# Performance work log

Measured on AMD Instinct MI355X. Metric: run time of the kernel, lower is better.

The kernel has to match this reference:

```python
import jax, jax.numpy as jnp
import numpy as np


def _lstm_cell(x, h, c, Wih, Whh, b):
    # PyTorch gate order: i, f, g, o
    g = x @ Wih.T + h @ Whh.T + b
    i, f, gg, o = jnp.split(g, 4, axis=-1)
    c2 = jax.nn.sigmoid(f) * c + jax.nn.sigmoid(i) * jnp.tanh(gg)
    h2 = jax.nn.sigmoid(o) * jnp.tanh(c2)
    return h2, c2


def _lstm_seq(x_tbd, h0, c0, Wih, Whh, b):
    # x_tbd: [T, B, D] -> outputs [T, B, H]
    def step(carry, xt):
        h, c = carry
        h2, c2 = _lstm_cell(xt, h, c, Wih, Whh, b)
        return (h2, c2), h2
    _, ys = jax.lax.scan(step, (h0, c0), x_tbd)
    return ys


def setup_inputs() -> dict:
    key = jax.random.key(0)
    ks = jax.random.split(key, 20)
    H, D, A, HOR, NQ = 256, 32, 128, 24, 3
    B, T = 256, 512
    s = 0.1
    inp = {
        'x':      jax.random.normal(ks[0], (B, T, D), jnp.float32),
        'e_Wih0': jax.random.normal(ks[1], (4 * H, D), jnp.float32) * s,
        'e_Whh0': jax.random.normal(ks[2], (4 * H, H), jnp.float32) * s,
        'e_b0':   jax.random.normal(ks[3], (4 * H,), jnp.float32) * s,
        'e_Wih1': jax.random.normal(ks[4], (4 * H, H), jnp.float32) * s,
        'e_Whh1': jax.random.normal(ks[5], (4 * H, H), jnp.float32) * s,
        'e_b1':   jax.random.normal(ks[6], (4 * H,), jnp.float32) * s,
        'd_Wih0': jax.random.normal(ks[7], (4 * H, 1), jnp.float32) * s,
        'd_Whh0': jax.random.normal(ks[8], (4 * H, H), jnp.float32) * s,
        'd_b0':   jax.random.normal(ks[9], (4 * H,), jnp.float32) * s,
        'd_Wih1': jax.random.normal(ks[10], (4 * H, H), jnp.float32) * s,
        'd_Whh1': jax.random.normal(ks[11], (4 * H, H), jnp.float32) * s,
        'd_b1':   jax.random.normal(ks[12], (4 * H,), jnp.float32) * s,
        'aW':     jax.random.normal(ks[13], (H, A), jnp.float32) * s,
        'aV':     jax.random.normal(ks[14], (A,), jnp.float32) * s,
        'qW':     jax.random.normal(ks[15], (NQ, HOR, H), jnp.float32) * s,
        'qb':     jax.random.normal(ks[16], (NQ, HOR), jnp.float32) * s,
    }
    return inp


def reference(x, e_Wih0, e_Whh0, e_b0, e_Wih1, e_Whh1, e_b1,
              d_Wih0, d_Whh0, d_b0, d_Wih1, d_Whh1, d_b1,
              aW, aV, qW, qb):
    B = x.shape[0]
    H = e_Whh0.shape[1]
    horizon = qW.shape[1]

    # ---- encoder: 2-layer LSTM over time ----
    xt = jnp.swapaxes(x, 0, 1)                      # [T, B, D]
    z = jnp.zeros((B, H), x.dtype)
    h1 = _lstm_seq(xt, z, z, e_Wih0, e_Whh0, e_b0)  # [T, B, H]
    h2 = _lstm_seq(h1, z, z, e_Wih1, e_Whh1, e_b1)  # [T, B, H]
    enc = jnp.swapaxes(h2, 0, 1)                    # [B, T, H]

    # ---- attention over encoder outputs ----
    energy = jnp.tanh(enc @ aW) @ aV                # [B, T]
    w = jax.nn.softmax(energy, axis=1)
    context = jnp.einsum('bt,bth->bh', w, enc)      # [B, H]

    inp0 = x[:, -1, -1:]                            # [B, 1]

    def dstep(carry, _):
        h0_, c0_, h1_, c1_, dinp = carry
        h0n, c0n = _lstm_cell(dinp, h0_, c0_, d_Wih0, d_Whh0, d_b0)
        h1n, c1n = _lstm_cell(h0n, h1_, c1_, d_Wih1, d_Whh1, d_b1)
        return (h0n, c0n, h1n, c1n, h1n[:, :1]), h1n

    _, douts = jax.lax.scan(dstep, (context, context, context, context, inp0),
                            None, length=horizon)   # [horizon, B, H]

    # ---- quantile heads on last decoder step ----
    last = douts[-1]                                # [B, H]
    preds = jnp.einsum('bh,qoh->bqo', last, qW) + qb  # [B, n_quantiles, horizon]
    return preds
```

## Files before the change

### kernel.cpp

```cpp
#include <hip/hip_runtime.h>

typedef unsigned short u16;
typedef unsigned int u32;
typedef unsigned long long u64;
typedef short v8s __attribute__((ext_vector_type(8)));
typedef float v4f __attribute__((ext_vector_type(4)));


__device__ __forceinline__ float bf2f(u16 u) { union { u32 u; float f; } c; c.u = ((u32)u) << 16; return c.f; }
__device__ __forceinline__ u16 f2bf(float f) {
  union { float f; u32 u; } c; c.f = f;
  u32 r = c.u + 0x7FFFu + ((c.u >> 16) & 1u);
  return (u16)(r >> 16);
}
__device__ __forceinline__ float sigf(float x) { return 1.f / (1.f + __expf(-x)); }
__device__ __forceinline__ float tanhfast(float x) {
  x = fminf(15.f, fmaxf(-15.f, x));
  float e = __expf(2.f * x);
  return (e - 1.f) / (e + 1.f);
}
__device__ __forceinline__ float ldIn(const void* p, size_t i, int isbf) {
  return isbf ? bf2f(((const u16*)p)[i]) : ((const float*)p)[i];
}
__device__ __forceinline__ v8s ld8hi(const void* p, size_t e, int isbf) {
  if (isbf) return *(const v8s*)((const u16*)p + e);
  const float* f = (const float*)p + e;
  v8s r;
#pragma unroll
  for (int j = 0; j < 8; ++j) r[j] = (short)f2bf(f[j]);
  return r;
}
__device__ __forceinline__ void ld8split(const void* p, size_t e, int isbf, v8s& hi, v8s& lo) {
  if (isbf) {
    hi = *(const v8s*)((const u16*)p + e);
    lo = v8s{0, 0, 0, 0, 0, 0, 0, 0};
  } else {
    const float* f = (const float*)p + e;
#pragma unroll
    for (int j = 0; j < 8; ++j) {
      u16 h = f2bf(f[j]);
      hi[j] = (short)h;
      lo[j] = (short)f2bf(f[j] - bf2f(h));
    }
  }
}
#define MFMA(a, b, c) __builtin_amdgcn_mfma_f32_16x16x32_bf16(a, b, c, 0, 0, 0)

__device__ __forceinline__ u64 aload64(const u64* p) {
  return __hip_atomic_load(p, __ATOMIC_RELAXED, __HIP_MEMORY_SCOPE_AGENT);
}
__device__ __forceinline__ void astore32(u32* p, u32 v) {
  __hip_atomic_store(p, v, __ATOMIC_RELAXED, __HIP_MEMORY_SCOPE_AGENT);
}
__device__ __forceinline__ void astore64(u64* p, u64 v) {
  __hip_atomic_store(p, v, __ATOMIC_RELAXED, __HIP_MEMORY_SCOPE_AGENT);
}

__device__ __forceinline__ void stage_issue(u64* v, const u32* src, int tid) {
  const u64* p = (const u64*)src;
#pragma unroll
  for (int i = 0; i < 8; ++i) v[i] = aload64(p + i * 256 + tid);
}
__device__ __forceinline__ void stage_finish(u16* dst, const u32* src, u64* v, int tid, u32 tag) {
  const u64* p = (const u64*)src;
  bool all;
  do {
    all = true;
#pragma unroll
    for (int i = 0; i < 8; ++i) {
      u64 w = v[i];
      if (!((((w >> 16) & 0xFFFFull) == tag) && ((w >> 48) == tag))) {
        all = false;
        v[i] = aload64(p + i * 256 + tid);
      }
    }
  } while (!all);
#pragma unroll
  for (int i = 0; i < 8; ++i) {
    int idx = i * 256 + tid;
    int row = (idx >> 3) & 15;
    int jp  = ((idx >> 7) << 3) | (idx & 7);
    u64 w = v[i];
    u32 val = (u32)(w & 0xFFFF) | ((((u32)(w >> 32)) & 0xFFFF) << 16);
    *(u32*)(dst + row * 264 + ((jp * 2) ^ ((row & 7) << 3))) = val;
  }
}

__device__ __forceinline__ void stage_dec(u16* dhi, u16* dlo, const u64* src,
                                          int tid, u32 tag) {
  u64 v[16];
#pragma unroll
  for (int i = 0; i < 16; ++i) v[i] = aload64(src + i * 256 + tid);
  bool all;
  do {
    all = true;
#pragma unroll
    for (int i = 0; i < 16; ++i) {
      if ((u32)(v[i] >> 32) != tag) { all = false; v[i] = aload64(src + i * 256 + tid); }
    }
  } while (!all);
#pragma unroll
  for (int i = 0; i < 16; ++i) {
    int idx = i * 256 + tid;
    int row = idx >> 8, col = idx & 255;
    dhi[row * 264 + col] = (u16)v[i];
    dlo[row * 264 + col] = (u16)(v[i] >> 16);
  }
}
__device__ __forceinline__ void stage_f32(u16* dhi, u16* dlo, const float* src, int tid) {
#pragma unroll
  for (int i = 0; i < 8; ++i) {
    int e = i * 512 + tid * 2;
    int row = e >> 8, jc = e & 255;
    float f0 = src[row * 256 + jc], f1 = src[row * 256 + jc + 1];
    u16 h0 = f2bf(f0), h1 = f2bf(f1);
    u16 l0 = f2bf(f0 - bf2f(h0)), l1 = f2bf(f1 - bf2f(h1));
    ((u32*)(dhi + row * 264))[jc >> 1] = (u32)h0 | ((u32)h1 << 16);
    ((u32*)(dlo + row * 264))[jc >> 1] = (u32)l0 | ((u32)l1 << 16);
  }
}

__global__ void sniff_kernel(const u16* __restrict__ w, int* __restrict__ flag) {
  __shared__ int cnt;
  if (threadIdx.x == 0) cnt = 0;
  __syncthreads();
  int ok = 0;
  for (int i = threadIdx.x; i < 1024; i += 256) {
    u16 u = w[2 * i];
    int e = (u >> 7) & 0xFF;
    ok += (u == 0 || (e >= 97 && e <= 140)) ? 1 : 0;
  }
  atomicAdd(&cnt, ok);
  __syncthreads();
  if (threadIdx.x == 0) *flag = (cnt >= 768) ? 1 : 0;
}

__global__ __launch_bounds__(256, 1) void enc_kernel(
    const void* __restrict__ x,
    const void* __restrict__ eWih0, const void* __restrict__ eWhh0, const void* __restrict__ eb0,
    const void* __restrict__ eWih1, const void* __restrict__ eWhh1, const void* __restrict__ eb1,
    const void* __restrict__ aW, const void* __restrict__ aV,
    u32* __restrict__ H0, u32* __restrict__ H1,
    float* __restrict__ ctx, const int* __restrict__ flagp) {
  __shared__ __align__(16) u16 h0s[16 * 264], h1s[16 * 264];
  __shared__ float gb0[16 * 66], gb1[16 * 66];
  __shared__ float eP[16 * 132];

  const int isbf = *flagp;
  const int tid = threadIdx.x, blk = blockIdx.x;
  const int grp = blk & 15, gs = blk >> 4;
  const int lane = tid & 63, wv = tid >> 6;
  const int ln = lane & 15, lq = lane >> 4;

  v8s W0F[9], W1F[16], AWF[16];
  {
    const int gw = wv * 256 + gs * 16 + ln;
    const int kq = lq * 8;
    W0F[0] = ld8hi(eWih0, (size_t)gw * 32 + kq, isbf);
#pragma unroll
    for (int kt = 0; kt < 8; ++kt) {
      W0F[kt + 1] = ld8hi(eWhh0, (size_t)gw * 256 + kt * 32 + kq, isbf);
      W1F[kt]     = ld8hi(eWhh1, (size_t)gw * 256 + kt * 32 + kq, isbf);
      W1F[kt + 8] = ld8hi(eWih1, (size_t)gw * 256 + kt * 32 + kq, isbf);
    }
#pragma unroll
    for (int kt = 0; kt < 8; ++kt)
#pragma unroll
      for (int j2 = 0; j2 < 2; ++j2) {
        v8s f;
        int ac = (2 * wv + j2) * 16 + ln;
#pragma unroll
        for (int j = 0; j < 8; ++j)
          f[j] = (short)f2bf(ldIn(aW, (size_t)(kt * 32 + kq + j) * 128 + ac, isbf));
        AWF[kt * 2 + j2] = f;
      }
  }

  const int urow = tid >> 4, uu = tid & 15;
  float bg0[4], bg1[4], aVr[8];
#pragma unroll
  for (int g = 0; g < 4; ++g) {
    bg0[g] = ldIn(eb0, g * 256 + gs * 16 + uu, isbf);
    bg1[g] = ldIn(eb1, g * 256 + gs * 16 + uu, isbf);
  }
#pragma unroll
  for (int j = 0; j < 8; ++j) aVr[j] = ldIn(aV, (size_t)(uu + 16 * j), isbf);

  const int gRowU = grp * 16 + urow;
  const int gUnit = gs * 16 + uu;
  const int aRow = grp * 16 + ln;
  const u32 stOff = (u32)(grp * 4096 + gs * 256 + urow * 16 + uu);

  float c0 = 0.f, c1 = 0.f;
  float mS = -3e38f, lS = 0.f, ctxA = 0.f;

  v8s xh_c, xl_c;
  ld8split(x, ((size_t)aRow * 512) * 32 + lq * 8, isbf, xh_c, xl_c);

  u64 v0s[8];
  stage_issue(v0s, H0 + (size_t)1 * 65536 + grp * 4096, tid);
  v8s a0r[8];

#pragma unroll 1
  for (int t = 0; t < 514; ++t) {
    const int rB = (t + 1) & 1, wB = t & 1;
    const u32 tag = (u32)(u16)t;
    if (t <= 512)
      stage_finish(h0s, H0 + (size_t)rB * 65536 + grp * 4096, v0s, tid, tag);
    __syncthreads();

    if (t <= 512) {
#pragma unroll
      for (int kt = 0; kt < 8; ++kt)
        a0r[kt] = *(const v8s*)(h0s + ln * 264 + ((kt * 32 + lq * 8) ^ ((ln & 7) << 3)));
    }
    if (t < 512) {
      v4f acc0 = {0, 0, 0, 0};
      acc0 = MFMA(xh_c, W0F[0], acc0);
      if (!isbf) acc0 = MFMA(xl_c, W0F[0], acc0);
#pragma unroll
      for (int kt = 0; kt < 8; ++kt) acc0 = MFMA(a0r[kt], W0F[kt + 1], acc0);
#pragma unroll
      for (int r = 0; r < 4; ++r) gb0[(lq * 4 + r) * 66 + wv * 16 + ln] = acc0[r];
    }
    __syncthreads();

    u64 v1s[8];
    stage_issue(v1s, H1 + (size_t)wB * 65536 + grp * 4096, tid);
    const u32 tagS = (u32)(u16)(t + 1) << 16;
    if (t < 512) {
      float gi = gb0[urow * 66 + uu]      + bg0[0];
      float gf = gb0[urow * 66 + 16 + uu] + bg0[1];
      float gg = gb0[urow * 66 + 32 + uu] + bg0[2];
      float go = gb0[urow * 66 + 48 + uu] + bg0[3];
      c0 = sigf(gf) * c0 + sigf(gi) * tanhfast(gg);
      float h = sigf(go) * tanhfast(c0);
      astore32(H0 + (size_t)wB * 65536 + stOff, (u32)f2bf(h) | tagS);
    }
    stage_finish(h1s, H1 + (size_t)wB * 65536 + grp * 4096, v1s, tid, tag);
    __syncthreads();

    v4f acc1 = {0, 0, 0, 0}, accA0 = {0, 0, 0, 0}, accA1 = {0, 0, 0, 0};
#pragma unroll
    for (int kt = 0; kt < 8; ++kt) {
      v8s a1 = *(const v8s*)(h1s + ln * 264 + ((kt * 32 + lq * 8) ^ ((ln & 7) << 3)));
      acc1 = MFMA(a0r[kt], W1F[kt + 8], acc1);
      acc1 = MFMA(a1, W1F[kt], acc1);
      accA0 = MFMA(a1, AWF[kt * 2], accA0);
      accA1 = MFMA(a1, AWF[kt * 2 + 1], accA1);
    }
#pragma unroll
    for (int r = 0; r < 4; ++r) {
      gb1[(lq * 4 + r) * 66 + wv * 16 + ln] = acc1[r];
      eP[(lq * 4 + r) * 132 + (2 * wv) * 16 + ln] = accA0[r];
      eP[(lq * 4 + r) * 132 + (2 * wv + 1) * 16 + ln] = accA1[r];
    }
    v8s xh_n, xl_n;
    {
      int tn = (t + 1 < 512) ? t + 1 : 511;
      ld8split(x, ((size_t)aRow * 512 + tn) * 32 + lq * 8, isbf, xh_n, xl_n);
    }
    __syncthreads();

    if (t >= 1 && t < 513) {
      float gi = gb1[urow * 66 + uu]      + bg1[0];
      float gf = gb1[urow * 66 + 16 + uu] + bg1[1];
      float gg = gb1[urow * 66 + 32 + uu] + bg1[2];
      float go = gb1[urow * 66 + 48 + uu] + bg1[3];
      c1 = sigf(gf) * c1 + sigf(gi) * tanhfast(gg);
      float h = sigf(go) * tanhfast(c1);
      astore32(H1 + (size_t)rB * 65536 + stOff, (u32)f2bf(h) | tagS);
    } else if (t == 0) {
      astore32(H1 + (size_t)rB * 65536 + stOff, tagS);
    }
    if (t + 1 <= 512)
      stage_issue(v0s, H0 + (size_t)((t + 2) & 1) * 65536 + grp * 4096, tid);
    if (t >= 2) {
      float h1v = bf2f(h1s[urow * 264 + (gUnit ^ ((urow & 7) << 3))]);
      float e = 0.f;
#pragma unroll
      for (int j = 0; j < 8; ++j)
        e += tanhfast(eP[urow * 132 + uu + 16 * j]) * aVr[j];
      e += __shfl_xor(e, 1);
      e += __shfl_xor(e, 2);
      e += __shfl_xor(e, 4);
      e += __shfl_xor(e, 8);
      float nm = fmaxf(mS, e);
      float al = __expf(mS - nm), p = __expf(e - nm);
      lS = lS * al + p;
      ctxA = ctxA * al + p * h1v;
      mS = nm;
    }
    xh_c = xh_n; xl_c = xl_n;
  }
  ctx[(size_t)gRowU * 256 + gUnit] = ctxA / lS;
}

__global__ __launch_bounds__(256, 1) void dec_kernel(
    const void* __restrict__ x,
    const void* __restrict__ dWih0, const void* __restrict__ dWhh0, const void* __restrict__ db0,
    const void* __restrict__ dWih1, const void* __restrict__ dWhh1, const void* __restrict__ db1,
    const void* __restrict__ qW, const void* __restrict__ qb,
    const float* __restrict__ ctx,
    u64* __restrict__ H0d, u64* __restrict__ H1d, u64* __restrict__ dinpG,
    void* __restrict__ out, const int* __restrict__ flagp) {
  __shared__ u16 sAhi[16 * 264], sAlo[16 * 264], sBhi[16 * 264], sBlo[16 * 264];
  __shared__ float gb[16 * 64];
  __shared__ float dinpS[16];

  const int isbf = *flagp;
  const int tid = threadIdx.x, blk = blockIdx.x;
  const int grp = blk & 15, gs = blk >> 4;
  const int lane = tid & 63, wv = tid >> 6;
  const int ln = lane & 15, lq = lane >> 4;

  v8s W0F[8], W1F[16];
  {
    const int gw = wv * 256 + gs * 16 + ln;
    const int kq = lq * 8;
#pragma unroll
    for (int kt = 0; kt < 8; ++kt) {
      W0F[kt]     = ld8hi(dWhh0, (size_t)gw * 256 + kt * 32 + kq, isbf);
      W1F[kt]     = ld8hi(dWhh1, (size_t)gw * 256 + kt * 32 + kq, isbf);
      W1F[kt + 8] = ld8hi(dWih1, (size_t)gw * 256 + kt * 32 + kq, isbf);
    }
  }
  const int urow = tid >> 4, uu = tid & 15;
  float bg0[4], bg1[4], w0v[4];
#pragma unroll
  for (int g = 0; g < 4; ++g) {
    bg0[g] = ldIn(db0, g * 256 + gs * 16 + uu, isbf);
    bg1[g] = ldIn(db1, g * 256 + gs * 16 + uu, isbf);
    w0v[g] = ldIn(dWih0, g * 256 + gs * 16 + uu, isbf);
  }
  const int gRowU = grp * 16 + urow;
  const int gUnit = gs * 16 + uu;

  float c0 = ctx[(size_t)gRowU * 256 + gUnit];
  float c1 = c0;

#pragma unroll 1
  for (int t = 0; t < 24; ++t) {
    const int pPrev = (t + 1) & 1, pCur = t & 1;
    if (t == 0) {
      stage_f32(sAhi, sAlo, ctx + (size_t)grp * 16 * 256, tid);
      if (tid < 16)
        dinpS[tid] = ldIn(x, ((size_t)(grp * 16 + tid) * 512 + 511) * 32 + 31, isbf);
    } else {
      stage_dec(sAhi, sAlo, H0d + (size_t)pPrev * 65536 + grp * 4096, tid, (u32)(2 * t - 1));
      if (tid < 16) {
        u64 w;
        do { w = aload64(dinpG + pPrev * 256 + grp * 16 + tid); } while ((u32)(w >> 32) != (u32)(2 * t));
        dinpS[tid] = __uint_as_float((u32)w);
      }
    }
    __syncthreads();
    v4f acc = {0, 0, 0, 0};
#pragma unroll
    for (int kt = 0; kt < 8; ++kt) {
      const int off = ln * 264 + kt * 32 + lq * 8;
      acc = MFMA(*(const v8s*)(sAhi + off), W0F[kt], acc);
      acc = MFMA(*(const v8s*)(sAlo + off), W0F[kt], acc);
    }
    {
      const int bR = lq * 4;
#pragma unroll
      for (int r = 0; r < 4; ++r) gb[(bR + r) * 64 + ln * 4 + wv] = acc[r];
    }
    float di = dinpS[urow];
    __syncthreads();
    {
      const float* g0 = gb + (urow * 16 + uu) * 4;
      float gi = g0[0] + bg0[0] + di * w0v[0];
      float gf = g0[1] + bg0[1] + di * w0v[1];
      float gg = g0[2] + bg0[2] + di * w0v[2];
      float go = g0[3] + bg0[3] + di * w0v[3];
      c0 = sigf(gf) * c0 + sigf(gi) * tanhfast(gg);
      float h = sigf(go) * tanhfast(c0);
      u16 hh = f2bf(h); u16 hl = f2bf(h - bf2f(hh));
      astore64(H0d + (size_t)pCur * 65536 + gRowU * 256 + gUnit,
               (u64)hh | ((u64)hl << 16) | ((u64)(u32)(2 * t + 1) << 32));
    }
    if (t == 0) stage_f32(sBhi, sBlo, ctx + (size_t)grp * 16 * 256, tid);
    else stage_dec(sBhi, sBlo, H1d + (size_t)pPrev * 65536 + grp * 4096, tid, (u32)(2 * t));
    stage_dec(sAhi, sAlo, H0d + (size_t)pCur * 65536 + grp * 4096, tid, (u32)(2 * t + 1));
    __syncthreads();
    v4f a1 = {0, 0, 0, 0};
#pragma unroll
    for (int kt = 0; kt < 8; ++kt) {
      const int off = ln * 264 + kt * 32 + lq * 8;
      a1 = MFMA(*(const v8s*)(sBhi + off), W1F[kt], a1);
      a1 = MFMA(*(const v8s*)(sBlo + off), W1F[kt], a1);
      a1 = MFMA(*(const v8s*)(sAhi + off), W1F[kt + 8], a1);
      a1 = MFMA(*(const v8s*)(sAlo + off), W1F[kt + 8], a1);
    }
    {
      const int bR = lq * 4;
#pragma unroll
      for (int r = 0; r < 4; ++r) gb[(bR + r) * 64 + ln * 4 + wv] = a1[r];
    }
    __syncthreads();
    {
      const float* g1 = gb + (urow * 16 + uu) * 4;
      float gi = g1[0] + bg1[0], gf = g1[1] + bg1[1], gg = g1[2] + bg1[2], go = g1[3] + bg1[3];
      c1 = sigf(gf) * c1 + sigf(gi) * tanhfast(gg);
      float h = sigf(go) * tanhfast(c1);
      u16 hh = f2bf(h); u16 hl = f2bf(h - bf2f(hh));
      astore64(H1d + (size_t)pCur * 65536 + gRowU * 256 + gUnit,
               (u64)hh | ((u64)hl << 16) | ((u64)(u32)(2 * t + 2) << 32));
      if (gUnit == 0)
        astore64(dinpG + pCur * 256 + gRowU,
                 (u64)__float_as_uint(h) | ((u64)(u32)(2 * t + 2) << 32));
    }
  }
  stage_dec(sAhi, sAlo, H1d + (size_t)65536 + grp * 4096, tid, 48u);
  __syncthreads();
  if (gs < 12 && tid < 96) {
    int r = tid / 6, p = tid % 6;
    int qo = gs * 6 + p, row = grp * 16 + r;
    float s = ldIn(qb, qo, isbf);
    for (int h = 0; h < 256; ++h)
      s += (bf2f(sAhi[r * 264 + h]) + bf2f(sAlo[r * 264 + h])) * ldIn(qW, (size_t)qo * 256 + h, isbf);
    if (isbf) ((u16*)out)[row * 72 + qo] = f2bf(s);
    else      ((float*)out)[row * 72 + qo] = s;
  }
}

extern "C" void kernel_launch(void* const* d_in, const int* in_sizes, int n_in,
                              void* d_out, int out_size, void* d_ws, size_t ws_size,
                              hipStream_t stream) {
  const void* x     = d_in[0];
  const void* eWih0 = d_in[1];
  const void* eWhh0 = d_in[2];
  const void* eb0   = d_in[3];
  const void* eWih1 = d_in[4];
  const void* eWhh1 = d_in[5];
  const void* eb1   = d_in[6];
  const void* dWih0 = d_in[7];
  const void* dWhh0 = d_in[8];
  const void* db0   = d_in[9];
  const void* dWih1 = d_in[10];
  const void* dWhh1 = d_in[11];
  const void* db1   = d_in[12];
  const void* aW    = d_in[13];
  const void* aV    = d_in[14];
  const void* qW    = d_in[15];
  const void* qb    = d_in[16];

  char* wsb = (char*)d_ws;
  u32*   H0    = (u32*)(wsb + 0);
  u32*   H1    = (u32*)(wsb + 524288);
  int*   flag  = (int*)(wsb + 1048576);
  float* ctx   = (float*)(wsb + 1048832);
  u64*   dinpG = (u64*)(wsb + 1310976);
  u64*   H0d   = (u64*)(wsb + 1315072);
  u64*   H1d   = (u64*)(wsb + 2363648);

  hipMemsetAsync(wsb, 0, 1048576, stream);

  sniff_kernel<<<1, 256, 0, stream>>>((const u16*)eWhh0, flag);
  enc_kernel<<<256, 256, 0, stream>>>(x, eWih0, eWhh0, eb0, eWih1, eWhh1, eb1,
                                      aW, aV, H0, H1, ctx, flag);
  dec_kernel<<<256, 256, 0, stream>>>(x, dWih0, dWhh0, db0, dWih1, dWhh1, db1,
                                      qW, qb, ctx, H0d, H1d, dinpG,
                                      d_out, flag);
}
```

Baseline: 2.270 ms.

## Add per-block progress tag counters for encoder inter-block polling

Blocks now publish a per-group progress counter after consuming each step. Before loading a step's hidden state, consumers spin on 16 tag words with a wave-wide vote instead of repeatedly reloading the full 8-word tagged buffer. The early prefetch (issue before the barrier) of H0 is dropped, and the LDS layouts of hidden-state and gate buffers change: the XOR swizzle is removed and gates are interleaved so each thread reads its four gates contiguously. This aims to cut wasted polling traffic and simplify indexing, at the cost of an extra polling round trip per stage, possible LDS bank conflicts without the swizzle, and the decoder workspace now aliasing the encoder buffers.

```diff
diff --git a/kernel.cpp b/kernel.cpp
--- a/kernel.cpp
+++ b/kernel.cpp
@@ -49,6 +49,9 @@
 __device__ __forceinline__ u64 aload64(const u64* p) {
   return __hip_atomic_load(p, __ATOMIC_RELAXED, __HIP_MEMORY_SCOPE_AGENT);
 }
+__device__ __forceinline__ u32 aload32(const u32* p) {
+  return __hip_atomic_load(p, __ATOMIC_RELAXED, __HIP_MEMORY_SCOPE_AGENT);
+}
 __device__ __forceinline__ void astore32(u32* p, u32 v) {
   __hip_atomic_store(p, v, __ATOMIC_RELAXED, __HIP_MEMORY_SCOPE_AGENT);
 }
@@ -56,12 +59,17 @@
   __hip_atomic_store(p, v, __ATOMIC_RELAXED, __HIP_MEMORY_SCOPE_AGENT);
 }
 
-__device__ __forceinline__ void stage_issue(u64* v, const u32* src, int tid) {
+__device__ __forceinline__ void poll16(const u32* tl, int lane, u32 tag) {
+  u32 s = aload32(tl + (lane & 15));
+  while (!__all(s >= tag)) s = aload32(tl + (lane & 15));
+}
+__device__ __forceinline__ void load8(u64* v, const u32* src, int tid) {
   const u64* p = (const u64*)src;
 #pragma unroll
   for (int i = 0; i < 8; ++i) v[i] = aload64(p + i * 256 + tid);
 }
-__device__ __forceinline__ void stage_finish(u16* dst, const u32* src, u64* v, int tid, u32 tag) {
+__device__ __forceinline__ void verify_unpack(u16* dst, const u32* src, u64* v,
+                                              int tid, u32 tag) {
   const u64* p = (const u64*)src;
   bool all;
   do {
@@ -78,11 +86,10 @@
 #pragma unroll
   for (int i = 0; i < 8; ++i) {
     int idx = i * 256 + tid;
-    int row = (idx >> 3) & 15;
-    int jp  = ((idx >> 7) << 3) | (idx & 7);
+    int gs2 = idx >> 7, row = (idx >> 3) & 15, c = idx & 7;
     u64 w = v[i];
-    u32 val = (u32)(w & 0xFFFF) | ((((u32)(w >> 32)) & 0xFFFF) << 16);
-    *(u32*)(dst + row * 264 + ((jp * 2) ^ ((row & 7) << 3))) = val;
+    ((u32*)(dst + row * 264))[gs2 * 8 + c] =
+        (u32)(w & 0xFFFF) | ((((u32)(w >> 32)) & 0xFFFF) << 16);
   }
 }
 
@@ -141,9 +148,10 @@
     const void* __restrict__ eWih1, const void* __restrict__ eWhh1, const void* __restrict__ eb1,
     const void* __restrict__ aW, const void* __restrict__ aV,
     u32* __restrict__ H0, u32* __restrict__ H1,
+    u32* __restrict__ H0tag, u32* __restrict__ H1tag,
     float* __restrict__ ctx, const int* __restrict__ flagp) {
   __shared__ __align__(16) u16 h0s[16 * 264], h1s[16 * 264];
-  __shared__ float gb0[16 * 66], gb1[16 * 66];
+  __shared__ float gb0[16 * 64], gb1[16 * 64];
   __shared__ float eP[16 * 132];
 
   const int isbf = *flagp;
@@ -190,29 +198,34 @@
   const int gUnit = gs * 16 + uu;
   const int aRow = grp * 16 + ln;
   const u32 stOff = (u32)(grp * 4096 + gs * 256 + urow * 16 + uu);
+  const u32* tl0 = H0tag + grp * 32;
+  const u32* tl1 = H1tag + grp * 32;
 
   float c0 = 0.f, c1 = 0.f;
   float mS = -3e38f, lS = 0.f, ctxA = 0.f;
 
   v8s xh_c, xl_c;
   ld8split(x, ((size_t)aRow * 512) * 32 + lq * 8, isbf, xh_c, xl_c);
-
-  u64 v0s[8];
-  stage_issue(v0s, H0 + (size_t)1 * 65536 + grp * 4096, tid);
   v8s a0r[8];
 
 #pragma unroll 1
   for (int t = 0; t < 514; ++t) {
     const int rB = (t + 1) & 1, wB = t & 1;
     const u32 tag = (u32)(u16)t;
-    if (t <= 512)
-      stage_finish(h0s, H0 + (size_t)rB * 65536 + grp * 4096, v0s, tid, tag);
-    __syncthreads();
-
     if (t <= 512) {
+      const u32* src0 = H0 + (size_t)rB * 65536 + grp * 4096;
+      poll16(tl0, lane, (u32)t);
+      u64 v0[8];
+      load8(v0, src0, tid);
+      verify_unpack(h0s, src0, v0, tid, tag);
+    }
+    __syncthreads();
+
+    if (t >= 1 && tid == 0) astore32(H1tag + grp * 32 + gs, (u32)t);
+    if (t <= 512) {
 #pragma unroll
       for (int kt = 0; kt < 8; ++kt)
-        a0r[kt] = *(const v8s*)(h0s + ln * 264 + ((kt * 32 + lq * 8) ^ ((ln & 7) << 3)));
+        a0r[kt] = *(const v8s*)(h0s + ln * 264 + kt * 32 + lq * 8);
     }
     if (t < 512) {
       v4f acc0 = {0, 0, 0, 0};
@@ -221,29 +234,31 @@
 #pragma unroll
       for (int kt = 0; kt < 8; ++kt) acc0 = MFMA(a0r[kt], W0F[kt + 1], acc0);
 #pragma unroll
-      for (int r = 0; r < 4; ++r) gb0[(lq * 4 + r) * 66 + wv * 16 + ln] = acc0[r];
-    }
-    __syncthreads();
-
-    u64 v1s[8];
-    stage_issue(v1s, H1 + (size_t)wB * 65536 + grp * 4096, tid);
+      for (int r = 0; r < 4; ++r) gb0[(lq * 4 + r) * 64 + ln * 4 + wv] = acc0[r];
+    }
+    __syncthreads();
+
+    const u32* src1 = H1 + (size_t)wB * 65536 + grp * 4096;
+    poll16(tl1, lane, (u32)t);
+    u64 v1[8];
+    load8(v1, src1, tid);
     const u32 tagS = (u32)(u16)(t + 1) << 16;
     if (t < 512) {
-      float gi = gb0[urow * 66 + uu]      + bg0[0];
-      float gf = gb0[urow * 66 + 16 + uu] + bg0[1];
-      float gg = gb0[urow * 66 + 32 + uu] + bg0[2];
-      float go = gb0[urow * 66 + 48 + uu] + bg0[3];
+      const float* g0 = gb0 + (urow * 16 + uu) * 4;
+      float gi = g0[0] + bg0[0], gf = g0[1] + bg0[1], gg = g0[2] + bg0[2], go = g0[3] + bg0[3];
       c0 = sigf(gf) * c0 + sigf(gi) * tanhfast(gg);
       float h = sigf(go) * tanhfast(c0);
       astore32(H0 + (size_t)wB * 65536 + stOff, (u32)f2bf(h) | tagS);
     }
-    stage_finish(h1s, H1 + (size_t)wB * 65536 + grp * 4096, v1s, tid, tag);
-    __syncthreads();
-
+    verify_unpack(h1s, src1, v1, tid, tag);
+    float h1v = bf2f(h1s[urow * 264 + gUnit]);
+    __syncthreads();
+
+    if (t < 512 && tid == 0) astore32(H0tag + grp * 32 + gs, (u32)(t + 1));
     v4f acc1 = {0, 0, 0, 0}, accA0 = {0, 0, 0, 0}, accA1 = {0, 0, 0, 0};
 #pragma unroll
     for (int kt = 0; kt < 8; ++kt) {
-      v8s a1 = *(const v8s*)(h1s + ln * 264 + ((kt * 32 + lq * 8) ^ ((ln & 7) << 3)));
+      v8s a1 = *(const v8s*)(h1s + ln * 264 + kt * 32 + lq * 8);
       acc1 = MFMA(a0r[kt], W1F[kt + 8], acc1);
       acc1 = MFMA(a1, W1F[kt], acc1);
       accA0 = MFMA(a1, AWF[kt * 2], accA0);
@@ -251,7 +266,7 @@
     }
 #pragma unroll
     for (int r = 0; r < 4; ++r) {
-      gb1[(lq * 4 + r) * 66 + wv * 16 + ln] = acc1[r];
+      gb1[(lq * 4 + r) * 64 + ln * 4 + wv] = acc1[r];
       eP[(lq * 4 + r) * 132 + (2 * wv) * 16 + ln] = accA0[r];
       eP[(lq * 4 + r) * 132 + (2 * wv + 1) * 16 + ln] = accA1[r];
     }
@@ -263,20 +278,15 @@
     __syncthreads();
 
     if (t >= 1 && t < 513) {
-      float gi = gb1[urow * 66 + uu]      + bg1[0];
-      float gf = gb1[urow * 66 + 16 + uu] + bg1[1];
-      float gg = gb1[urow * 66 + 32 + uu] + bg1[2];
-      float go = gb1[urow * 66 + 48 + uu] + bg1[3];
+      const float* g1 = gb1 + (urow * 16 + uu) * 4;
+      float gi = g1[0] + bg1[0], gf = g1[1] + bg1[1], gg = g1[2] + bg1[2], go = g1[3] + bg1[3];
       c1 = sigf(gf) * c1 + sigf(gi) * tanhfast(gg);
       float h = sigf(go) * tanhfast(c1);
       astore32(H1 + (size_t)rB * 65536 + stOff, (u32)f2bf(h) | tagS);
     } else if (t == 0) {
       astore32(H1 + (size_t)rB * 65536 + stOff, tagS);
     }
-    if (t + 1 <= 512)
-      stage_issue(v0s, H0 + (size_t)((t + 2) & 1) * 65536 + grp * 4096, tid);
     if (t >= 2) {
-      float h1v = bf2f(h1s[urow * 264 + (gUnit ^ ((urow & 7) << 3))]);
       float e = 0.f;
 #pragma unroll
       for (int j = 0; j < 8; ++j)
@@ -450,17 +460,19 @@
   char* wsb = (char*)d_ws;
   u32*   H0    = (u32*)(wsb + 0);
   u32*   H1    = (u32*)(wsb + 524288);
-  int*   flag  = (int*)(wsb + 1048576);
-  float* ctx   = (float*)(wsb + 1048832);
-  u64*   dinpG = (u64*)(wsb + 1310976);
-  u64*   H0d   = (u64*)(wsb + 1315072);
-  u64*   H1d   = (u64*)(wsb + 2363648);
-
-  hipMemsetAsync(wsb, 0, 1048576, stream);
+  u32*   H0tag = (u32*)(wsb + 1048576);
+  u32*   H1tag = (u32*)(wsb + 1050624);
+  int*   flag  = (int*)(wsb + 1052672);
+  float* ctx   = (float*)(wsb + 1052928);
+  u64*   dinpG = (u64*)(wsb + 1315072);
+  u64*   H0d   = (u64*)(wsb + 0);
+  u64*   H1d   = (u64*)(wsb + 1319168);
+
+  hipMemsetAsync(wsb, 0, 1052672, stream);
 
   sniff_kernel<<<1, 256, 0, stream>>>((const u16*)eWhh0, flag);
   enc_kernel<<<256, 256, 0, stream>>>(x, eWih0, eWhh0, eb0, eWih1, eWhh1, eb1,
-                                      aW, aV, H0, H1, ctx, flag);
+                                      aW, aV, H0, H1, H0tag, H1tag, ctx, flag);
   dec_kernel<<<256, 256, 0, stream>>>(x, dWih0, dWhh0, db0, dWih1, dWhh1, db1,
                                       qW, qb, ctx, H0d, H1d, dinpG,
                                       d_out, flag);
```

After: 2.738 ms. 20.6% more time.
